# Performance work log

Hardware: AMD Instinct MI355X
Metric: run time of the kernel (lower is better)

## Reference

```python
import jax, jax.numpy as jnp
import numpy as np

QUERY_DIM = 1024
HIDDEN_DIM = 1024


def setup_inputs() -> dict:
    key = jax.random.key(0)
    k1, k2, k3, k4 = jax.random.split(key, 4)
    query = jax.random.normal(k1, (8, 2048, QUERY_DIM), dtype=jnp.float32)
    info = jax.random.normal(k2, (8, 2048, HIDDEN_DIM), dtype=jnp.float32)
    # nn.Linear params: weight [out, in], bias [out]
    bound = 1.0 / np.sqrt(QUERY_DIM)
    W = jax.random.uniform(k3, (HIDDEN_DIM, QUERY_DIM), jnp.float32, -bound, bound)
    b = jax.random.uniform(k4, (HIDDEN_DIM,), jnp.float32, -bound, bound)
    return {"query": query, "info": info, "W": W, "b": b}


def reference(query, info, W, b):
    # Eval mode: dropout is identity.
    # projected query: [B, S, hidden]
    q = jnp.einsum("bsq,hq->bsh", query, W) + b
    # unscaled attention scores over info rows: [B, S, M]
    scores = jax.nn.softmax(jnp.einsum("bsh,bmh->bsm", q, info), axis=-1)
    # weighted sum of info: [B, S, hidden]
    return jnp.einsum("bsm,bmh->bsh", scores, info)
```

## Files before the change

kernel.cpp:

```cpp
#include <hip/hip_runtime.h>

#define DEVI __device__ __forceinline__

typedef __attribute__((ext_vector_type(4))) float f32x4;
typedef __attribute__((ext_vector_type(8))) short bf16x8;

typedef const unsigned __attribute__((address_space(1))) as1_u32;
typedef unsigned __attribute__((address_space(3))) as3_u32;

DEVI unsigned fbits(float x){ union{float f;unsigned u;} v; v.f=x; return v.u; }
DEVI float bitsf(unsigned u){ union{unsigned u;float f;} v; v.u=u; return v.f; }
DEVI short bf_rne(float x){ unsigned u=fbits(x); u += 0x7fffu + ((u>>16)&1u); return (short)(u>>16); }

DEVI unsigned pack_hi2(unsigned u0, unsigned u1){
#if __has_builtin(__builtin_amdgcn_perm)
  return __builtin_amdgcn_perm(u1, u0, 0x07060302u);
#else
  return (u0 >> 16) | (u1 & 0xffff0000u);
#endif
}
DEVI unsigned pack_rne2(float a, float b){
  return (unsigned)(unsigned short)bf_rne(a) | ((unsigned)(unsigned short)bf_rne(b) << 16);
}

DEVI void gload16(const short* g, short* s){
  __builtin_amdgcn_global_load_lds((as1_u32*)g, (as3_u32*)s, 16, 0, 0);
}

#define SBAR() { __builtin_amdgcn_sched_barrier(0); asm volatile("" ::: "memory"); \
                 __builtin_amdgcn_s_barrier(); __builtin_amdgcn_sched_barrier(0); }

#define MF(a,b,c) __builtin_amdgcn_mfma_f32_16x16x32_bf16(a,b,c,0,0,0)
#define MROW(M, x) \
  acc[M][0] = MF(x, bb0, acc[M][0]); \
  acc[M][1] = MF(x, bb1, acc[M][1]); \
  acc[M][2] = MF(x, bb2, acc[M][2]); \
  acc[M][3] = MF(x, bb3, acc[M][3]);

__global__ __launch_bounds__(256)
void k_split(const float* __restrict__ in, short* __restrict__ hi,
             short* __restrict__ lo, const long n4)
{
  long i = (long)blockIdx.x*256 + threadIdx.x;
  const long stride = (long)gridDim.x*256;
  for (; i < n4; i += stride){
    const float4 v = ((const float4*)in)[i];
    const unsigned u0=fbits(v.x), u1=fbits(v.y), u2=fbits(v.z), u3=fbits(v.w);
    ((uint2*)hi)[i] = make_uint2(pack_hi2(u0,u1), pack_hi2(u2,u3));
    const float l0 = v.x - bitsf(u0 & 0xffff0000u);
    const float l1 = v.y - bitsf(u1 & 0xffff0000u);
    const float l2 = v.z - bitsf(u2 & 0xffff0000u);
    const float l3 = v.w - bitsf(u3 & 0xffff0000u);
    ((uint2*)lo)[i] = make_uint2(pack_rne2(l0,l1), pack_rne2(l2,l3));
  }
}

template<bool BIAS, bool SPLIT_OUT>
__global__ __launch_bounds__(512, 2)
void k_gemm3(const short* __restrict__ Ah, const short* __restrict__ Al,
             const short* __restrict__ Bh, const short* __restrict__ Bl,
             void* __restrict__ Cv, const float* __restrict__ bias,
             const int K, const int lda, const int ldb, const int ldc,
             const long sAz, const long sBz, const long sCz, const int loOff)
{
  __shared__ short LDS[65536];

  const int tid = threadIdx.x;
  const int w = tid >> 6, l = tid & 63;
  const int wr = w >> 2, wc = w & 3;
  const int fr = l & 15, h4 = l >> 4;
  const long bz = blockIdx.z;

  const int nwg = gridDim.x * gridDim.y;
  const int xy  = blockIdx.y * gridDim.x + blockIdx.x;
  const int q8  = nwg >> 3;
  const int sw  = (xy & 7) * q8 + (xy >> 3);
  const int bx  = sw % gridDim.x;
  const int by  = sw / gridDim.x;

  const size_t aOff = (size_t)bz*sAz + (size_t)bx*256*lda;
  const size_t bOff = (size_t)bz*sBz + (size_t)by*256*ldb;

  const int c0 = w*64 + l, c1 = c0 + 512;
  const int k0 = ((c0 & 3) ^ ((c0 >> 3) & 3)) * 8;
  const int k1 = ((c1 & 3) ^ ((c1 >> 3) & 3)) * 8;
  const size_t a0 = (size_t)(c0 >> 2)*lda + k0;
  const size_t a1 = (size_t)(c1 >> 2)*lda + k1;
  const size_t b0 = (size_t)(c0 >> 2)*ldb + k0;
  const size_t b1 = (size_t)(c1 >> 2)*ldb + k1;
  const int dS0 = w*512, dS1 = 4096 + w*512;

  const int cswz = (h4 ^ ((fr >> 1) & 3)) << 3;
  const int rbA = (wr*128 + fr)*32 + cswz;
  const int rbB = 16384 + (wc*64 + fr)*32 + cswz;

  f32x4 acc[8][4];
#pragma unroll
  for (int m = 0; m < 8; ++m)
#pragma unroll
    for (int n = 0; n < 4; ++n){ acc[m][n][0]=0.f; acc[m][n][1]=0.f; acc[m][n][2]=0.f; acc[m][n][3]=0.f; }

  const short* pAh = Ah + aOff;
  const short* pAl = Al + aOff;
  const short* pBh = Bh + bOff;
  const short* pBl = Bl + bOff;

  gload16(pAh + a0, LDS + dS0);
  gload16(pAh + a1, LDS + dS1);
  gload16(pBh + b0, LDS + 16384 + dS0);
  gload16(pBh + b1, LDS + 16384 + dS1);
  gload16(pAl + a0, LDS + 8192 + dS0);
  gload16(pAl + a1, LDS + 8192 + dS1);
  gload16(pBl + b0, LDS + 24576 + dS0);
  gload16(pBl + b1, LDS + 24576 + dS1);
  pAh += 32; pAl += 32; pBh += 32; pBl += 32;
  asm volatile("s_waitcnt vmcnt(0)" ::: "memory");
  SBAR();

#define STEP3(CO, PF)                                                        \
{                                                                            \
  const short* pA = LDS + (CO) + rbA;                                        \
  const short* pB = LDS + (CO) + rbB;                                        \
  short* dst = LDS + ((CO) ^ 32768);                                         \
  bf16x8 ah0,ah1,ah2,ah3,ah4,ah5,ah6,ah7, bb0,bb1,bb2,bb3;                   \
   \
  if (PF){ gload16(pAh + a0, dst + dS0);                                     \
           gload16(pAh + a1, dst + dS1);                                     \
           gload16(pBh + b0, dst + 16384 + dS0);                             \
           gload16(pBh + b1, dst + 16384 + dS1);                             \
           gload16(pAl + a0, dst + 8192 + dS0);                              \
           gload16(pAl + a1, dst + 8192 + dS1);                              \
           gload16(pBl + b0, dst + 24576 + dS0);                             \
           gload16(pBl + b1, dst + 24576 + dS1);                             \
           pAh += 32; pAl += 32; pBh += 32; pBl += 32; }                     \
  __builtin_amdgcn_sched_barrier(0);                                         \
                                                            \
  bb0 = *(const bf16x8*)(pB);                                                \
  bb1 = *(const bf16x8*)(pB + 512);                                          \
  bb2 = *(const bf16x8*)(pB + 1024);                                         \
  bb3 = *(const bf16x8*)(pB + 1536);                                         \
  ah0 = *(const bf16x8*)(pA);                                                \
  ah1 = *(const bf16x8*)(pA + 512);                                          \
  ah2 = *(const bf16x8*)(pA + 1024);                                         \
  ah3 = *(const bf16x8*)(pA + 1536);                                         \
  ah4 = *(const bf16x8*)(pA + 2048);                                         \
  ah5 = *(const bf16x8*)(pA + 2560);                                         \
  ah6 = *(const bf16x8*)(pA + 3072);                                         \
  ah7 = *(const bf16x8*)(pA + 3584);                                         \
  __builtin_amdgcn_s_setprio(1);                                             \
  MROW(0,ah0) MROW(1,ah1) MROW(2,ah2) MROW(3,ah3)                            \
  MROW(4,ah4) MROW(5,ah5) MROW(6,ah6) MROW(7,ah7)                            \
  __builtin_amdgcn_s_setprio(0);                                             \
                                                            \
  {                                                                          \
    bf16x8 al0 = *(const bf16x8*)(pA + 8192);                                \
    bf16x8 al1 = *(const bf16x8*)(pA + 8192 + 512);                          \
    bf16x8 al2 = *(const bf16x8*)(pA + 8192 + 1024);                         \
    bf16x8 al3 = *(const bf16x8*)(pA + 8192 + 1536);                         \
    bf16x8 al4 = *(const bf16x8*)(pA + 8192 + 2048);                         \
    bf16x8 al5 = *(const bf16x8*)(pA + 8192 + 2560);                         \
    bf16x8 al6 = *(const bf16x8*)(pA + 8192 + 3072);                         \
    bf16x8 al7 = *(const bf16x8*)(pA + 8192 + 3584);                         \
    __builtin_amdgcn_s_setprio(1);                                           \
    MROW(0,al0) MROW(1,al1) MROW(2,al2) MROW(3,al3)                          \
    MROW(4,al4) MROW(5,al5) MROW(6,al6) MROW(7,al7)                          \
    __builtin_amdgcn_s_setprio(0);                                           \
  }                                                                          \
                                   \
  bb0 = *(const bf16x8*)(pB + 8192);                                         \
  bb1 = *(const bf16x8*)(pB + 8192 + 512);                                   \
  bb2 = *(const bf16x8*)(pB + 8192 + 1024);                                  \
  bb3 = *(const bf16x8*)(pB + 8192 + 1536);                                  \
  __builtin_amdgcn_s_setprio(1);                                             \
  MROW(0,ah0) MROW(1,ah1) MROW(2,ah2) MROW(3,ah3)                            \
  MROW(4,ah4) MROW(5,ah5) MROW(6,ah6) MROW(7,ah7)                            \
  __builtin_amdgcn_s_setprio(0);                                             \
                                           \
  asm volatile("s_waitcnt vmcnt(0)" ::: "memory");                           \
  SBAR();                                                                    \
}

  const int nk = K >> 5;
#pragma unroll 1
  for (int it = 0; it < nk - 2; it += 2){
    STEP3(0,     1)
    STEP3(32768, 1)
  }
  STEP3(0,     1)
  STEP3(32768, 0)

#undef STEP3

  const int rr = h4*4;
  if constexpr (SPLIT_OUT){
    short* Ch = (short*)Cv + (size_t)bz*sCz
              + (size_t)(bx*256 + wr*128)*ldc + by*256 + wc*64;
    short* Cl = Ch + loOff;
#pragma unroll
    for (int n = 0; n < 4; ++n){
      const int col = n*16 + fr;
      const float bv = BIAS ? bias[by*256 + wc*64 + col] : 0.f;
#pragma unroll
      for (int m = 0; m < 8; ++m)
#pragma unroll
        for (int j = 0; j < 4; ++j){
          const float v = acc[m][n][j] + bv;
          const unsigned uh = fbits(v) & 0xffff0000u;
          const size_t idx = (size_t)(m*16 + rr + j)*ldc + col;
          Ch[idx] = (short)(uh >> 16);
          Cl[idx] = bf_rne(v - bitsf(uh));
        }
    }
  } else {
    float* C = (float*)Cv + (size_t)bz*sCz
             + (size_t)(bx*256 + wr*128)*ldc + by*256 + wc*64;
#pragma unroll
    for (int n = 0; n < 4; ++n){
      const int col = n*16 + fr;
      const float bv = BIAS ? bias[by*256 + wc*64 + col] : 0.f;
#pragma unroll
      for (int m = 0; m < 8; ++m)
#pragma unroll
        for (int j = 0; j < 4; ++j)
          C[(size_t)(m*16 + rr + j)*ldc + col] = acc[m][n][j] + bv;
    }
  }
}

__global__ __launch_bounds__(512, 2)
void k_gemm1(const short* __restrict__ Ah, const short* __restrict__ Bh,
             void* __restrict__ Cv,
             const int K, const int lda, const int ldb, const int ldc,
             const long sAz, const long sBz, const long sCz)
{
  __shared__ short LDS[65536];

  const int tid = threadIdx.x;
  const int w = tid >> 6, l = tid & 63;
  const int wr = w >> 2, wc = w & 3;
  const int fr = l & 15, h4 = l >> 4;
  const long bz = blockIdx.z;

  const int nwg = gridDim.x * gridDim.y;
  const int xy  = blockIdx.y * gridDim.x + blockIdx.x;
  const int q8  = nwg >> 3;
  const int sw  = (xy & 7) * q8 + (xy >> 3);
  const int bx  = sw % gridDim.x;
  const int by  = sw / gridDim.x;

  const size_t aOff = (size_t)bz*sAz + (size_t)bx*256*lda;
  const size_t bOff = (size_t)bz*sBz + (size_t)by*256*ldb;

  const int sch = (((l & 7) ^ ((l >> 3) & 7)) << 3);
  const int rA0 = wr*128 + (w & 3)*8 + (l >> 3);
  int aoffg[4];
#pragma unroll
  for (int q2 = 0; q2 < 4; ++q2) aoffg[q2] = (rA0 + 32*q2)*lda;
  const int rB0 = wc*64 + (w >> 2)*8 + (l >> 3);
  int boffg[4];
#pragma unroll
  for (int j2 = 0; j2 < 4; ++j2) boffg[j2] = (rB0 + 16*j2)*ldb;
  const int dAu = wr*8192 + (w & 3)*512;
  const int dBu = 16384 + wc*4096 + (w >> 2)*512;

  const int rbA = (wr*128 + fr)*64;
  const int rbB = 16384 + (wc*64 + fr)*64;
  const int c08 = ((h4     ) ^ (l & 7)) << 3;
  const int c18 = ((h4 + 4 ) ^ (l & 7)) << 3;

  f32x4 acc[8][4];
#pragma unroll
  for (int m = 0; m < 8; ++m)
#pragma unroll
    for (int n = 0; n < 4; ++n){ acc[m][n][0]=0.f; acc[m][n][1]=0.f; acc[m][n][2]=0.f; acc[m][n][3]=0.f; }

  const short* Asrc = Ah + aOff + sch;
  const short* Bsrc = Bh + bOff + sch;

  {
    short* dB0 = LDS + dBu;
    short* dA0 = LDS + dAu;
    gload16(Bsrc + boffg[0], dB0);
    gload16(Bsrc + boffg[1], dB0 + 1024);
    gload16(Bsrc + boffg[2], dB0 + 2048);
    gload16(Bsrc + boffg[3], dB0 + 3072);
    gload16(Asrc + aoffg[0], dA0);
    gload16(Asrc + aoffg[1], dA0 + 2048);
    gload16(Asrc + aoffg[2], dA0 + 4096);
    gload16(Asrc + aoffg[3], dA0 + 6144);
  }
  Asrc += 64; Bsrc += 64;
  asm volatile("s_waitcnt vmcnt(0)" ::: "memory");
  SBAR();

#define TILE(CO, PF)                                                         \
{                                                                            \
  const short* pA = LDS + (CO) + rbA;                                        \
  const short* pB = LDS + (CO) + rbB;                                        \
  short* dAp = LDS + ((CO)^32768) + dAu;                                     \
  short* dBp = LDS + ((CO)^32768) + dBu;                                     \
  bf16x8 aA,aB,aC,aD, bb0,bb1,bb2,bb3;                                       \
  if (PF){ gload16(Bsrc + boffg[0], dBp);                                    \
           gload16(Bsrc + boffg[1], dBp + 1024);                             \
           gload16(Bsrc + boffg[2], dBp + 2048);                             \
           gload16(Bsrc + boffg[3], dBp + 3072);                             \
           gload16(Asrc + aoffg[0], dAp);                                    \
           gload16(Asrc + aoffg[1], dAp + 2048);                             \
           gload16(Asrc + aoffg[2], dAp + 4096);                             \
           gload16(Asrc + aoffg[3], dAp + 6144);                             \
           Asrc += 64; Bsrc += 64; }                                         \
  __builtin_amdgcn_sched_barrier(0);                                         \
                                                                    \
  bb0 = *(const bf16x8*)(pB +        c08);                                   \
  bb1 = *(const bf16x8*)(pB + 1024 + c08);                                   \
  bb2 = *(const bf16x8*)(pB + 2048 + c08);                                   \
  bb3 = *(const bf16x8*)(pB + 3072 + c08);                                   \
  aA  = *(const bf16x8*)(pA +        c08);                                   \
  aB  = *(const bf16x8*)(pA + 1024 + c08);                                   \
  aC  = *(const bf16x8*)(pA + 2048 + c08);                                   \
  aD  = *(const bf16x8*)(pA + 3072 + c08);                                   \
  __builtin_amdgcn_s_setprio(1);                                             \
  MROW(0,aA) MROW(1,aB) MROW(2,aC) MROW(3,aD)                                \
  __builtin_amdgcn_s_setprio(0);                                             \
  aA = *(const bf16x8*)(pA + 4096 + c08);                                    \
  aB = *(const bf16x8*)(pA + 5120 + c08);                                    \
  aC = *(const bf16x8*)(pA + 6144 + c08);                                    \
  aD = *(const bf16x8*)(pA + 7168 + c08);                                    \
  __builtin_amdgcn_s_setprio(1);                                             \
  MROW(4,aA) MROW(5,aB) MROW(6,aC) MROW(7,aD)                                \
  __builtin_amdgcn_s_setprio(0);                                             \
                                                                    \
  bb0 = *(const bf16x8*)(pB +        c18);                                   \
  bb1 = *(const bf16x8*)(pB + 1024 + c18);                                   \
  bb2 = *(const bf16x8*)(pB + 2048 + c18);                                   \
  bb3 = *(const bf16x8*)(pB + 3072 + c18);                                   \
  aA  = *(const bf16x8*)(pA +        c18);                                   \
  aB  = *(const bf16x8*)(pA + 1024 + c18);                                   \
  aC  = *(const bf16x8*)(pA + 2048 + c18);                                   \
  aD  = *(const bf16x8*)(pA + 3072 + c18);                                   \
  __builtin_amdgcn_s_setprio(1);                                             \
  MROW(0,aA) MROW(1,aB) MROW(2,aC) MROW(3,aD)                                \
  __builtin_amdgcn_s_setprio(0);                                             \
  aA = *(const bf16x8*)(pA + 4096 + c18);                                    \
  aB = *(const bf16x8*)(pA + 5120 + c18);                                    \
  aC = *(const bf16x8*)(pA + 6144 + c18);                                    \
  aD = *(const bf16x8*)(pA + 7168 + c18);                                    \
  __builtin_amdgcn_s_setprio(1);                                             \
  MROW(4,aA) MROW(5,aB) MROW(6,aC) MROW(7,aD)                                \
  __builtin_amdgcn_s_setprio(0);                                             \
  asm volatile("s_waitcnt vmcnt(0)" ::: "memory");                           \
  SBAR();                                                                    \
}

  const int nkt = K >> 6;
#pragma unroll 1
  for (int it = 0; it < nkt - 2; it += 2){
    TILE(0,     1)
    TILE(32768, 1)
  }
  TILE(0,     1)
  TILE(32768, 0)

#undef TILE

  const int rr = h4*4;
  float* C = (float*)Cv + (size_t)bz*sCz
           + (size_t)(bx*256 + wr*128)*ldc + by*256 + wc*64;
#pragma unroll
  for (int n = 0; n < 4; ++n){
    const int col = n*16 + fr;
#pragma unroll
    for (int m = 0; m < 8; ++m)
#pragma unroll
      for (int j = 0; j < 4; ++j)
        C[(size_t)(m*16 + rr + j)*ldc + col] = acc[m][n][j];
  }
}

__global__ __launch_bounds__(256)
void k_prep_info(const float* __restrict__ V, short* __restrict__ hi,
                 short* __restrict__ lo, short* __restrict__ T,
                 const int MM, const int DD, const long sVz, const long sTz)
{
  __shared__ float t[64][65];
  const float* Vb = V + (long)blockIdx.z*sVz;
  short* hb = hi + (long)blockIdx.z*sVz;
  short* lb = lo + (long)blockIdx.z*sVz;
  short* Tb = T  + (long)blockIdx.z*sTz;
  const int m0 = blockIdx.x*64, d0 = blockIdx.y*64;
  const int tid = threadIdx.x;
#pragma unroll
  for (int i = 0; i < 4; ++i){
    const int c = tid + 256*i;
    const int r = c >> 4, c4 = (c & 15)*4;
    const float4 v = *(const float4*)(Vb + (size_t)(m0 + r)*DD + d0 + c4);
    t[r][c4+0]=v.x; t[r][c4+1]=v.y; t[r][c4+2]=v.z; t[r][c4+3]=v.w;
    const unsigned u0=fbits(v.x), u1=fbits(v.y), u2=fbits(v.z), u3=fbits(v.w);
    const size_t gi = (size_t)(m0 + r)*DD + d0 + c4;
    *(uint2*)(hb + gi) = make_uint2(pack_hi2(u0,u1), pack_hi2(u2,u3));
    const float l0 = v.x - bitsf(u0 & 0xffff0000u);
    const float l1 = v.y - bitsf(u1 & 0xffff0000u);
    const float l2 = v.z - bitsf(u2 & 0xffff0000u);
    const float l3 = v.w - bitsf(u3 & 0xffff0000u);
    *(uint2*)(lb + gi) = make_uint2(pack_rne2(l0,l1), pack_rne2(l2,l3));
  }
  __syncthreads();
#pragma unroll
  for (int i = 0; i < 4; ++i){
    const int c = tid + 256*i;
    const int d = c >> 4, m4 = (c & 15)*4;
    short4 o;
    o.x = bf_rne(t[m4+0][d]); o.y = bf_rne(t[m4+1][d]);
    o.z = bf_rne(t[m4+2][d]); o.w = bf_rne(t[m4+3][d]);
    *(short4*)(Tb + (size_t)(d0 + d)*MM + m0 + m4) = o;
  }
}

__global__ __launch_bounds__(256)
void k_softmax_rows(float* __restrict__ Sb, const long sz)
{
  float* row = Sb + (long)blockIdx.y*sz + (long)blockIdx.x*2048;
  short* prow = (short*)row;
  const int tid = threadIdx.x;
  const int lane = tid & 63, wid = tid >> 6;

  const float4 v0 = *(const float4*)(row + tid*4);
  const float4 v1 = *(const float4*)(row + 1024 + tid*4);
  float x[8] = {v0.x, v0.y, v0.z, v0.w, v1.x, v1.y, v1.z, v1.w};

  float mx = x[0];
#pragma unroll
  for (int j = 1; j < 8; ++j) mx = fmaxf(mx, x[j]);
#pragma unroll
  for (int off = 32; off; off >>= 1) mx = fmaxf(mx, __shfl_xor(mx, off));

  __shared__ float red[8];
  if (lane == 0) red[wid] = mx;
  __syncthreads();
  mx = fmaxf(fmaxf(red[0], red[1]), fmaxf(red[2], red[3]));

  float e[8]; float s = 0.f;
#pragma unroll
  for (int j = 0; j < 8; ++j){ e[j] = __expf(x[j] - mx); s += e[j]; }
#pragma unroll
  for (int off = 32; off; off >>= 1) s += __shfl_xor(s, off);
  if (lane == 0) red[4 + wid] = s;
  __syncthreads();
  s = (red[4] + red[5]) + (red[6] + red[7]);
  const float inv = 1.0f / s;

  *(uint2*)(prow + tid*4)        = make_uint2(pack_rne2(e[0]*inv, e[1]*inv), pack_rne2(e[2]*inv, e[3]*inv));
  *(uint2*)(prow + 1024 + tid*4) = make_uint2(pack_rne2(e[4]*inv, e[5]*inv), pack_rne2(e[6]*inv, e[7]*inv));
}

extern "C" void kernel_launch(void* const* d_in, const int* in_sizes, int n_in,
                              void* d_out, int out_size, void* d_ws, size_t ws_size,
                              hipStream_t stream)
{
  const float* query = (const float*)d_in[0];
  const float* info  = (const float*)d_in[1];
  const float* Wm    = (const float*)d_in[2];
  const float* bias  = (const float*)d_in[3];
  float* out = (float*)d_out;

  const int B = 8, S = 2048, M = 2048, D = 1024;
  const size_t PB = (size_t)S * D;

  short* info_hi = (short*)d_ws;
  short* info_lo = info_hi + 16777216;
  short* infoT   = info_lo + 16777216;
  short* W_hi    = infoT   + 16777216;
  short* W_lo    = W_hi    + 1048576;
  float* Sbuf    = (float*)(W_lo + 1048576);
  const size_t sb = (size_t)S * M * sizeof(float);
  size_t avail = ws_size > 104857600ull ? ws_size - 104857600ull : 0;
  int nchunk = (int)(avail / sb); if (nchunk > 8) nchunk = 8; if (nchunk < 1) nchunk = 1;

  short* q_s = (short*)d_out;
  const long qBz = 2*(long)PB;
  const int  qLo = (int)PB;

  k_split<<<1024, 256, 0, stream>>>(Wm, W_hi, W_lo, (long)(D*D/4));

  int nb = 2*nchunk; if (nb > 8) nb = 8;
  for (int q0 = 0; q0 < B; q0 += nb){
    const int cur = (q0 + nb <= B) ? nb : (B - q0);
    short* qt_hi = (short*)Sbuf;
    short* qt_lo = qt_hi + (size_t)cur*PB;
    k_split<<<2048, 256, 0, stream>>>(query + (size_t)q0*PB, qt_hi, qt_lo,
                                      (long)((size_t)cur*PB/4));
    k_gemm3<true, true><<<dim3(S/256, D/256, cur), 512, 0, stream>>>(
        qt_hi, qt_lo, W_hi, W_lo, q_s + (size_t)q0*qBz, bias,
        D, D, D, D, (long)PB, 0L, qBz, qLo);
  }

  k_prep_info<<<dim3(M/64, D/64, B), 256, 0, stream>>>(
      info, info_hi, info_lo, infoT, M, D, (long)PB, (long)PB);

  for (int b0 = 0; b0 < B; b0 += nchunk){
    const int cur = (b0 + nchunk <= B) ? nchunk : (B - b0);

    const short* qh = q_s + (size_t)b0*qBz;
    k_gemm3<false, false><<<dim3(S/256, M/256, cur), 512, 0, stream>>>(
        qh, qh + qLo, info_hi + (size_t)b0*PB, info_lo + (size_t)b0*PB,
        Sbuf, nullptr, D, D, D, M, qBz, (long)PB, (long)S*M, 0);

    k_softmax_rows<<<dim3(S, cur), 256, 0, stream>>>(Sbuf, (long)S*M);

    k_gemm1<<<dim3(S/256, D/256, cur), 512, 0, stream>>>(
        (const short*)Sbuf, infoT + (size_t)b0*PB,
        out + (size_t)b0*PB, M, 2*M, M, D,
        (long)(2*(size_t)S*M), (long)PB, (long)S*D);
  }
}
```

Measured before the change: 444.8 us.

## Replace double-buffered LDS prefetch with single-buffer load-then-compute loop

Both GEMM kernels drop the ping-pong LDS double buffer, halving shared memory to 64KB per block. The global loads for the next K tile are now issued only after compute on the current tile and a barrier, then waited on before the next compute. Global memory latency is no longer hidden behind MFMA work within a block. The intent is presumably higher occupancy or lower LDS pressure, with an extra barrier per step as the cost.

```diff
diff --git a/kernel.cpp b/kernel.cpp
--- a/kernel.cpp
+++ b/kernel.cpp
@@ -63,7 +63,7 @@
              const int K, const int lda, const int ldb, const int ldc,
              const long sAz, const long sBz, const long sCz, const int loOff)
 {
-  __shared__ short LDS[65536];
+  __shared__ short LDS[32768];
 
   const int tid = threadIdx.x;
   const int w = tid >> 6, l = tid & 63;
@@ -117,79 +117,65 @@
   asm volatile("s_waitcnt vmcnt(0)" ::: "memory");
   SBAR();
 
-#define STEP3(CO, PF)                                                        \
-{                                                                            \
-  const short* pA = LDS + (CO) + rbA;                                        \
-  const short* pB = LDS + (CO) + rbB;                                        \
-  short* dst = LDS + ((CO) ^ 32768);                                         \
-  bf16x8 ah0,ah1,ah2,ah3,ah4,ah5,ah6,ah7, bb0,bb1,bb2,bb3;                   \
-   \
-  if (PF){ gload16(pAh + a0, dst + dS0);                                     \
-           gload16(pAh + a1, dst + dS1);                                     \
-           gload16(pBh + b0, dst + 16384 + dS0);                             \
-           gload16(pBh + b1, dst + 16384 + dS1);                             \
-           gload16(pAl + a0, dst + 8192 + dS0);                              \
-           gload16(pAl + a1, dst + 8192 + dS1);                              \
-           gload16(pBl + b0, dst + 24576 + dS0);                             \
-           gload16(pBl + b1, dst + 24576 + dS1);                             \
-           pAh += 32; pAl += 32; pBh += 32; pBl += 32; }                     \
-  __builtin_amdgcn_sched_barrier(0);                                         \
-                                                            \
-  bb0 = *(const bf16x8*)(pB);                                                \
-  bb1 = *(const bf16x8*)(pB + 512);                                          \
-  bb2 = *(const bf16x8*)(pB + 1024);                                         \
-  bb3 = *(const bf16x8*)(pB + 1536);                                         \
-  ah0 = *(const bf16x8*)(pA);                                                \
-  ah1 = *(const bf16x8*)(pA + 512);                                          \
-  ah2 = *(const bf16x8*)(pA + 1024);                                         \
-  ah3 = *(const bf16x8*)(pA + 1536);                                         \
-  ah4 = *(const bf16x8*)(pA + 2048);                                         \
-  ah5 = *(const bf16x8*)(pA + 2560);                                         \
-  ah6 = *(const bf16x8*)(pA + 3072);                                         \
-  ah7 = *(const bf16x8*)(pA + 3584);                                         \
-  __builtin_amdgcn_s_setprio(1);                                             \
-  MROW(0,ah0) MROW(1,ah1) MROW(2,ah2) MROW(3,ah3)                            \
-  MROW(4,ah4) MROW(5,ah5) MROW(6,ah6) MROW(7,ah7)                            \
-  __builtin_amdgcn_s_setprio(0);                                             \
-                                                            \
-  {                                                                          \
-    bf16x8 al0 = *(const bf16x8*)(pA + 8192);                                \
-    bf16x8 al1 = *(const bf16x8*)(pA + 8192 + 512);                          \
-    bf16x8 al2 = *(const bf16x8*)(pA + 8192 + 1024);                         \
-    bf16x8 al3 = *(const bf16x8*)(pA + 8192 + 1536);                         \
-    bf16x8 al4 = *(const bf16x8*)(pA + 8192 + 2048);                         \
-    bf16x8 al5 = *(const bf16x8*)(pA + 8192 + 2560);                         \
-    bf16x8 al6 = *(const bf16x8*)(pA + 8192 + 3072);                         \
-    bf16x8 al7 = *(const bf16x8*)(pA + 8192 + 3584);                         \
-    __builtin_amdgcn_s_setprio(1);                                           \
-    MROW(0,al0) MROW(1,al1) MROW(2,al2) MROW(3,al3)                          \
-    MROW(4,al4) MROW(5,al5) MROW(6,al6) MROW(7,al7)                          \
-    __builtin_amdgcn_s_setprio(0);                                           \
-  }                                                                          \
-                                   \
-  bb0 = *(const bf16x8*)(pB + 8192);                                         \
-  bb1 = *(const bf16x8*)(pB + 8192 + 512);                                   \
-  bb2 = *(const bf16x8*)(pB + 8192 + 1024);                                  \
-  bb3 = *(const bf16x8*)(pB + 8192 + 1536);                                  \
-  __builtin_amdgcn_s_setprio(1);                                             \
-  MROW(0,ah0) MROW(1,ah1) MROW(2,ah2) MROW(3,ah3)                            \
-  MROW(4,ah4) MROW(5,ah5) MROW(6,ah6) MROW(7,ah7)                            \
-  __builtin_amdgcn_s_setprio(0);                                             \
-                                           \
-  asm volatile("s_waitcnt vmcnt(0)" ::: "memory");                           \
-  SBAR();                                                                    \
-}
-
   const int nk = K >> 5;
 #pragma unroll 1
-  for (int it = 0; it < nk - 2; it += 2){
-    STEP3(0,     1)
-    STEP3(32768, 1)
-  }
-  STEP3(0,     1)
-  STEP3(32768, 0)
-
-#undef STEP3
+  for (int it = 0; it < nk; ++it){
+    const short* pA = LDS + rbA;
+    const short* pB = LDS + rbB;
+    bf16x8 ah0,ah1,ah2,ah3,ah4,ah5,ah6,ah7, bb0,bb1,bb2,bb3;
+    bb0 = *(const bf16x8*)(pB);
+    bb1 = *(const bf16x8*)(pB + 512);
+    bb2 = *(const bf16x8*)(pB + 1024);
+    bb3 = *(const bf16x8*)(pB + 1536);
+    ah0 = *(const bf16x8*)(pA);
+    ah1 = *(const bf16x8*)(pA + 512);
+    ah2 = *(const bf16x8*)(pA + 1024);
+    ah3 = *(const bf16x8*)(pA + 1536);
+    ah4 = *(const bf16x8*)(pA + 2048);
+    ah5 = *(const bf16x8*)(pA + 2560);
+    ah6 = *(const bf16x8*)(pA + 3072);
+    ah7 = *(const bf16x8*)(pA + 3584);
+    __builtin_amdgcn_s_setprio(1);
+    MROW(0,ah0) MROW(1,ah1) MROW(2,ah2) MROW(3,ah3)
+    MROW(4,ah4) MROW(5,ah5) MROW(6,ah6) MROW(7,ah7)
+    __builtin_amdgcn_s_setprio(0);
+    {
+      bf16x8 al0 = *(const bf16x8*)(pA + 8192);
+      bf16x8 al1 = *(const bf16x8*)(pA + 8192 + 512);
+      bf16x8 al2 = *(const bf16x8*)(pA + 8192 + 1024);
+      bf16x8 al3 = *(const bf16x8*)(pA + 8192 + 1536);
+      bf16x8 al4 = *(const bf16x8*)(pA + 8192 + 2048);
+      bf16x8 al5 = *(const bf16x8*)(pA + 8192 + 2560);
+      bf16x8 al6 = *(const bf16x8*)(pA + 8192 + 3072);
+      bf16x8 al7 = *(const bf16x8*)(pA + 8192 + 3584);
+      __builtin_amdgcn_s_setprio(1);
+      MROW(0,al0) MROW(1,al1) MROW(2,al2) MROW(3,al3)
+      MROW(4,al4) MROW(5,al5) MROW(6,al6) MROW(7,al7)
+      __builtin_amdgcn_s_setprio(0);
+    }
+    bb0 = *(const bf16x8*)(pB + 8192);
+    bb1 = *(const bf16x8*)(pB + 8192 + 512);
+    bb2 = *(const bf16x8*)(pB + 8192 + 1024);
+    bb3 = *(const bf16x8*)(pB + 8192 + 1536);
+    __builtin_amdgcn_s_setprio(1);
+    MROW(0,ah0) MROW(1,ah1) MROW(2,ah2) MROW(3,ah3)
+    MROW(4,ah4) MROW(5,ah5) MROW(6,ah6) MROW(7,ah7)
+    __builtin_amdgcn_s_setprio(0);
+    SBAR();
+    if (it + 1 < nk){
+      gload16(pAh + a0, LDS + dS0);
+      gload16(pAh + a1, LDS + dS1);
+      gload16(pBh + b0, LDS + 16384 + dS0);
+      gload16(pBh + b1, LDS + 16384 + dS1);
+      gload16(pAl + a0, LDS + 8192 + dS0);
+      gload16(pAl + a1, LDS + 8192 + dS1);
+      gload16(pBl + b0, LDS + 24576 + dS0);
+      gload16(pBl + b1, LDS + 24576 + dS1);
+      pAh += 32; pAl += 32; pBh += 32; pBl += 32;
+      asm volatile("s_waitcnt vmcnt(0)" ::: "memory");
+      SBAR();
+    }
+  }
 
   const int rr = h4*4;
   if constexpr (SPLIT_OUT){
@@ -233,7 +219,7 @@
              const int K, const int lda, const int ldb, const int ldc,
              const long sAz, const long sBz, const long sCz)
 {
-  __shared__ short LDS[65536];
+  __shared__ short LDS[32768];
 
   const int tid = threadIdx.x;
   const int w = tid >> 6, l = tid & 63;
@@ -293,75 +279,65 @@
   asm volatile("s_waitcnt vmcnt(0)" ::: "memory");
   SBAR();
 
-#define TILE(CO, PF)                                                         \
-{                                                                            \
-  const short* pA = LDS + (CO) + rbA;                                        \
-  const short* pB = LDS + (CO) + rbB;                                        \
-  short* dAp = LDS + ((CO)^32768) + dAu;                                     \
-  short* dBp = LDS + ((CO)^32768) + dBu;                                     \
-  bf16x8 aA,aB,aC,aD, bb0,bb1,bb2,bb3;                                       \
-  if (PF){ gload16(Bsrc + boffg[0], dBp);                                    \
-           gload16(Bsrc + boffg[1], dBp + 1024);                             \
-           gload16(Bsrc + boffg[2], dBp + 2048);                             \
-           gload16(Bsrc + boffg[3], dBp + 3072);                             \
-           gload16(Asrc + aoffg[0], dAp);                                    \
-           gload16(Asrc + aoffg[1], dAp + 2048);                             \
-           gload16(Asrc + aoffg[2], dAp + 4096);                             \
-           gload16(Asrc + aoffg[3], dAp + 6144);                             \
-           Asrc += 64; Bsrc += 64; }                                         \
-  __builtin_amdgcn_sched_barrier(0);                                         \
-                                                                    \
-  bb0 = *(const bf16x8*)(pB +        c08);                                   \
-  bb1 = *(const bf16x8*)(pB + 1024 + c08);                                   \
-  bb2 = *(const bf16x8*)(pB + 2048 + c08);                                   \
-  bb3 = *(const bf16x8*)(pB + 3072 + c08);                                   \
-  aA  = *(const bf16x8*)(pA +        c08);                                   \
-  aB  = *(const bf16x8*)(pA + 1024 + c08);                                   \
-  aC  = *(const bf16x8*)(pA + 2048 + c08);                                   \
-  aD  = *(const bf16x8*)(pA + 3072 + c08);                                   \
-  __builtin_amdgcn_s_setprio(1);                                             \
-  MROW(0,aA) MROW(1,aB) MROW(2,aC) MROW(3,aD)                                \
-  __builtin_amdgcn_s_setprio(0);                                             \
-  aA = *(const bf16x8*)(pA + 4096 + c08);                                    \
-  aB = *(const bf16x8*)(pA + 5120 + c08);                                    \
-  aC = *(const bf16x8*)(pA + 6144 + c08);                                    \
-  aD = *(const bf16x8*)(pA + 7168 + c08);                                    \
-  __builtin_amdgcn_s_setprio(1);                                             \
-  MROW(4,aA) MROW(5,aB) MROW(6,aC) MROW(7,aD)                                \
-  __builtin_amdgcn_s_setprio(0);                                             \
-                                                                    \
-  bb0 = *(const bf16x8*)(pB +        c18);                                   \
-  bb1 = *(const bf16x8*)(pB + 1024 + c18);                                   \
-  bb2 = *(const bf16x8*)(pB + 2048 + c18);                                   \
-  bb3 = *(const bf16x8*)(pB + 3072 + c18);                                   \
-  aA  = *(const bf16x8*)(pA +        c18);                                   \
-  aB  = *(const bf16x8*)(pA + 1024 + c18);                                   \
-  aC  = *(const bf16x8*)(pA + 2048 + c18);                                   \
-  aD  = *(const bf16x8*)(pA + 3072 + c18);                                   \
-  __builtin_amdgcn_s_setprio(1);                                             \
-  MROW(0,aA) MROW(1,aB) MROW(2,aC) MROW(3,aD)                                \
-  __builtin_amdgcn_s_setprio(0);                                             \
-  aA = *(const bf16x8*)(pA + 4096 + c18);                                    \
-  aB = *(const bf16x8*)(pA + 5120 + c18);                                    \
-  aC = *(const bf16x8*)(pA + 6144 + c18);                                    \
-  aD = *(const bf16x8*)(pA + 7168 + c18);                                    \
-  __builtin_amdgcn_s_setprio(1);                                             \
-  MROW(4,aA) MROW(5,aB) MROW(6,aC) MROW(7,aD)                                \
-  __builtin_amdgcn_s_setprio(0);                                             \
-  asm volatile("s_waitcnt vmcnt(0)" ::: "memory");                           \
-  SBAR();                                                                    \
-}
-
   const int nkt = K >> 6;
 #pragma unroll 1
-  for (int it = 0; it < nkt - 2; it += 2){
-    TILE(0,     1)
-    TILE(32768, 1)
-  }
-  TILE(0,     1)
-  TILE(32768, 0)
-
-#undef TILE
+  for (int it = 0; it < nkt; ++it){
+    const short* pA = LDS + rbA;
+    const short* pB = LDS + rbB;
+    bf16x8 aA,aB,aC,aD, bb0,bb1,bb2,bb3;
+    bb0 = *(const bf16x8*)(pB +        c08);
+    bb1 = *(const bf16x8*)(pB + 1024 + c08);
+    bb2 = *(const bf16x8*)(pB + 2048 + c08);
+    bb3 = *(const bf16x8*)(pB + 3072 + c08);
+    aA  = *(const bf16x8*)(pA +        c08);
+    aB  = *(const bf16x8*)(pA + 1024 + c08);
+    aC  = *(const bf16x8*)(pA + 2048 + c08);
+    aD  = *(const bf16x8*)(pA + 3072 + c08);
+    __builtin_amdgcn_s_setprio(1);
+    MROW(0,aA) MROW(1,aB) MROW(2,aC) MROW(3,aD)
+    __builtin_amdgcn_s_setprio(0);
+    aA = *(const bf16x8*)(pA + 4096 + c08);
+    aB = *(const bf16x8*)(pA + 5120 + c08);
+    aC = *(const bf16x8*)(pA + 6144 + c08);
+    aD = *(const bf16x8*)(pA + 7168 + c08);
+    __builtin_amdgcn_s_setprio(1);
+    MROW(4,aA) MROW(5,aB) MROW(6,aC) MROW(7,aD)
+    __builtin_amdgcn_s_setprio(0);
+    bb0 = *(const bf16x8*)(pB +        c18);
+    bb1 = *(const bf16x8*)(pB + 1024 + c18);
+    bb2 = *(const bf16x8*)(pB + 2048 + c18);
+    bb3 = *(const bf16x8*)(pB + 3072 + c18);
+    aA  = *(const bf16x8*)(pA +        c18);
+    aB  = *(const bf16x8*)(pA + 1024 + c18);
+    aC  = *(const bf16x8*)(pA + 2048 + c18);
+    aD  = *(const bf16x8*)(pA + 3072 + c18);
+    __builtin_amdgcn_s_setprio(1);
+    MROW(0,aA) MROW(1,aB) MROW(2,aC) MROW(3,aD)
+    __builtin_amdgcn_s_setprio(0);
+    aA = *(const bf16x8*)(pA + 4096 + c18);
+    aB = *(const bf16x8*)(pA + 5120 + c18);
+    aC = *(const bf16x8*)(pA + 6144 + c18);
+    aD = *(const bf16x8*)(pA + 7168 + c18);
+    __builtin_amdgcn_s_setprio(1);
+    MROW(4,aA) MROW(5,aB) MROW(6,aC) MROW(7,aD)
+    __builtin_amdgcn_s_setprio(0);
+    SBAR();
+    if (it + 1 < nkt){
+      short* dB0 = LDS + dBu;
+      short* dA0 = LDS + dAu;
+      gload16(Bsrc + boffg[0], dB0);
+      gload16(Bsrc + boffg[1], dB0 + 1024);
+      gload16(Bsrc + boffg[2], dB0 + 2048);
+      gload16(Bsrc + boffg[3], dB0 + 3072);
+      gload16(Asrc + aoffg[0], dA0);
+      gload16(Asrc + aoffg[1], dA0 + 2048);
+      gload16(Asrc + aoffg[2], dA0 + 4096);
+      gload16(Asrc + aoffg[3], dA0 + 6144);
+      Asrc += 64; Bsrc += 64;
+      asm volatile("s_waitcnt vmcnt(0)" ::: "memory");
+      SBAR();
+    }
+  }
 
   const int rr = h4*4;
   float* C = (float*)Cv + (size_t)bz*sCz
```

New measurement: 543.5 us. +22.2%, slower.
